# Optimization experiments

Measured on AMD Instinct MI355X. Metric: run time of the kernel, lower is better.

## Reference

```python
import jax, jax.numpy as jnp
import numpy as np

SCALE = 1.0 / 4.0      # alpha / dim
MULTIPLIER = 1.0

def _act(h):
    return jax.nn.gelu(h, approximate=False)  # torch nn.GELU(approximate='none')

def setup_inputs() -> dict:
    key = jax.random.key(0)
    ks = jax.random.split(key, 9)
    B, T, D = 64, 77, 768
    N, R = 1024, 4
    return {
        "x":     jax.random.normal(ks[0], (B, T, D), jnp.float32),
        "W_org": jax.random.normal(ks[1], (D, D), jnp.float32) * 0.02,
        "b_org": jax.random.normal(ks[2], (D,), jnp.float32) * 0.02,
        "w1":    jax.random.normal(ks[3], (N, D, R), jnp.float32) * 0.02,
        "b1":    jax.random.normal(ks[4], (N, R), jnp.float32) * 0.02,
        "mid_w": jax.random.normal(ks[5], (N, R, R), jnp.float32) * 0.02,
        "mid_b": jax.random.normal(ks[6], (N, R), jnp.float32) * 0.02,
        "w_out": jax.random.normal(ks[7], (N, R, D), jnp.float32) * 0.02,
        "b_out": jax.random.normal(ks[8], (N, D), jnp.float32) * 0.02,
    }

def reference(x, W_org, b_org, w1, b1, mid_w, mid_b, w_out, b_out):
    # per-concept low-rank MLP: h in [B, T, N, R]
    h = jnp.einsum('btd,ndh->btnh', x, w1) + b1[None, None]
    h = _act(h)
    # repeated 'h' in 'nhh' takes the diagonal of mid_w (elementwise scale),
    # exactly matching torch.einsum semantics in the source.
    h = jnp.einsum('btnh,nhh->btnh', h, mid_w) + mid_b[None, None]
    h = _act(h)
    # fuse out-projection with sum over concepts: sum_n (h_n @ w_out_n) + sum_n b_out_n
    up = jnp.einsum('btnh,nhd->btd', h, w_out) + jnp.sum(b_out, axis=0)
    org = x @ W_org.T + b_org
    return org + up * (MULTIPLIER * SCALE)
```

## Files before the change

### kernel.cpp

```cpp
#include <hip/hip_runtime.h>
#include <hip/hip_bf16.h>

#define M_TOK 4928
#define M_PAD 5120
#define D_DIM 768
#define NR    4096
#define K_CAT 4864
#define KT_ALL 152

typedef __bf16 bf16;
typedef __attribute__((ext_vector_type(8))) __bf16 bf16x8;
typedef __attribute__((ext_vector_type(4))) float f32x4;
typedef __attribute__((address_space(1))) uint32_t gu32;
typedef __attribute__((address_space(3))) uint32_t su32;

__device__ __forceinline__ float gelu_fast(float v) {
  float p = v * v;
  float u = v * fmaf(0.07135481283f, p, 1.595769122f);
  float e = __expf(-u);
  return v * __builtin_amdgcn_rcpf(1.0f + e);
}

__device__ __forceinline__ int xcd_swizzle(int orig, int nwg) {
  const int q = nwg >> 3, r = nwg & 7;
  const int x = orig & 7, rest = orig >> 3;
  return (x < r ? x * (q + 1) : r * (q + 1) + (x - r) * q) + rest;
}


__global__ __launch_bounds__(256) void k_prep_x(const float* __restrict__ x,
                                                bf16* __restrict__ Xb) {
  int idx = (blockIdx.x * 256 + threadIdx.x) * 4;
  if (idx >= M_PAD * D_DIM) return;
  int m = idx / D_DIM;
  union { uint2 u; bf16 h[4]; } o;
  if (m < M_TOK) {
    float4 v = *(const float4*)(x + idx);
    o.h[0] = (bf16)v.x; o.h[1] = (bf16)v.y; o.h[2] = (bf16)v.z; o.h[3] = (bf16)v.w;
  } else {
    o.h[0] = o.h[1] = o.h[2] = o.h[3] = (bf16)0.0f;
  }
  *(uint2*)(Xb + idx) = o.u;
}

__global__ __launch_bounds__(256) void k_prep_w1t(const float* __restrict__ w1,
                                                  bf16* __restrict__ W1t) {
  int idx = (blockIdx.x * 256 + threadIdx.x) * 4;
  if (idx >= NR * D_DIM) return;
  int j = idx / D_DIM, d0 = idx % D_DIM;
  int n = j >> 2, r = j & 3;
  const float* src = w1 + n * (D_DIM * 4) + r;
  union { uint2 u; bf16 h[4]; } o;
#pragma unroll
  for (int i = 0; i < 4; ++i) o.h[i] = (bf16)src[(d0 + i) * 4];
  *(uint2*)(W1t + idx) = o.u;
}

__global__ __launch_bounds__(256) void k_prep_w2t_t(const float* __restrict__ w_out,
                                                    bf16* __restrict__ W2t) {
  __shared__ float S[64 * 65];
  const int bk = blockIdx.x & 63, bd = blockIdx.x >> 6;
  const int k0 = bk * 64, d0 = bd * 64;
  const int tr = threadIdx.x >> 4;
  const int tc = (threadIdx.x & 15) * 4;
#pragma unroll
  for (int p = 0; p < 4; ++p) {
    const int kr = tr + p * 16;
    float4 v = *(const float4*)(w_out + (size_t)(k0 + kr) * D_DIM + d0 + tc);
    S[kr * 65 + tc + 0] = v.x; S[kr * 65 + tc + 1] = v.y;
    S[kr * 65 + tc + 2] = v.z; S[kr * 65 + tc + 3] = v.w;
  }
  __syncthreads();
#pragma unroll
  for (int p = 0; p < 4; ++p) {
    const int dr = tr + p * 16;
    union { uint2 u; bf16 h[4]; } o;
#pragma unroll
    for (int i = 0; i < 4; ++i) o.h[i] = (bf16)(0.25f * S[(tc + i) * 65 + dr]);
    *(uint2*)(W2t + (size_t)(d0 + dr) * K_CAT + k0 + tc) = o.u;
  }
}

__global__ __launch_bounds__(256) void k_prep_w2t_org(const float* __restrict__ W_org,
                                                      bf16* __restrict__ W2t) {
  int idx = (blockIdx.x * 256 + threadIdx.x) * 4;
  if (idx >= D_DIM * D_DIM) return;
  int d = idx / D_DIM, c = idx % D_DIM;
  float4 v = *(const float4*)(W_org + idx);
  union { uint2 u; bf16 h[4]; } o;
  o.h[0] = (bf16)v.x; o.h[1] = (bf16)v.y; o.h[2] = (bf16)v.z; o.h[3] = (bf16)v.w;
  *(uint2*)(W2t + (size_t)d * K_CAT + NR + c) = o.u;
}

__global__ __launch_bounds__(256) void k_bias_partial(const float* __restrict__ b_out,
                                                      float* __restrict__ partial) {
  int b = blockIdx.x;
  for (int d = threadIdx.x; d < D_DIM; d += 256) {
    float s = 0.0f;
    for (int n = b * 32; n < b * 32 + 32; ++n) s += b_out[n * D_DIM + d];
    partial[b * D_DIM + d] = s;
  }
}

__global__ __launch_bounds__(256) void k_bias_final(const float* __restrict__ partial,
                                                    const float* __restrict__ b_org,
                                                    float* __restrict__ bias_total) {
  int d = blockIdx.x * 256 + threadIdx.x;
  if (d >= D_DIM) return;
  float s = 0.0f;
#pragma unroll
  for (int b = 0; b < 32; ++b) s += partial[b * D_DIM + d];
  bias_total[d] = b_org[d] + 0.25f * s;
}


__device__ __forceinline__ int swz_slot(int kg, int lr) {
  return (kg ^ ((lr >> 1) & 3)) << 3;
}

__device__ __forceinline__ void stage_tile4(const bf16* g, int ld, int row0, int col0,
                                            bf16* lds) {
  const int lane = threadIdx.x & 63;
  const int wave = threadIdx.x >> 6;
  const int src_slot = (lane & 3) ^ ((lane >> 3) & 3);
#pragma unroll
  for (int c = 0; c < 2; ++c) {
    const int chunk = wave * 2 + c;
    const int row = row0 + chunk * 16 + (lane >> 2);
    const bf16* gp = g + (size_t)row * ld + col0 + (src_slot << 3);
    __builtin_amdgcn_global_load_lds((gu32*)gp, (su32*)(lds + chunk * 512), 16, 0, 0);
  }
}

__device__ __forceinline__ void stage_unit8(const bf16* g, int ld, int row0, int col0,
                                            bf16* lds) {
  const int lane = threadIdx.x & 63;
  const int wave = threadIdx.x >> 6;
  const int src_slot = (lane & 3) ^ ((lane >> 3) & 3);
#pragma unroll
  for (int c = 0; c < 2; ++c) {
    const int chunk = wave * 2 + c;
    const int row = row0 + chunk * 16 + (lane >> 2);
    const bf16* gp = g + (size_t)row * ld + col0 + (src_slot << 3);
    __builtin_amdgcn_global_load_lds((gu32*)gp, (su32*)(lds + chunk * 512), 16, 0, 0);
  }
}

#define TILE_E (128 * 32)

#define PIPE_LOOP(KT0, KT1, STAGE_PAIR, BODY)                                   \
  {                                                                             \
    STAGE_PAIR(KT0, 0);                                                         \
    STAGE_PAIR((KT0) + 1, 1);                                                   \
    int ra = 0;                                                                 \
    for (int kt = (KT0); kt < (KT1); ++kt) {                                    \
      if (kt + 1 < (KT1)) { asm volatile("s_waitcnt vmcnt(4)" ::: "memory"); }  \
      else                { asm volatile("s_waitcnt vmcnt(0)" ::: "memory"); }  \
      asm volatile("s_barrier" ::: "memory");                                   \
      const int rs = ra + 2 >= 3 ? ra - 1 : ra + 2;                             \
      BODY(ra);                                                                 \
      if (kt + 2 < (KT1)) STAGE_PAIR(kt + 2, rs);                               \
      ra = (ra + 1 == 3) ? 0 : ra + 1;                                          \
    }                                                                           \
  }

__global__ __launch_bounds__(256) void k_gemm1(const bf16* __restrict__ Xb,
                                               const bf16* __restrict__ W1t,
                                               bf16* __restrict__ H2,
                                               const float* __restrict__ b1,
                                               const float* __restrict__ midw,
                                               const float* __restrict__ midb) {
  __shared__ bf16 As[3][TILE_E];
  __shared__ bf16 Bs[3][TILE_E];
  const int wgid = xcd_swizzle(blockIdx.x, 40 * 32);
  const int bmt = wgid >> 5;
  const int bnt = wgid & 31;
  const int m0 = bmt * 128, n0 = bnt * 128;
  const int lane = threadIdx.x & 63;
  const int wave = threadIdx.x >> 6;
  const int wm = wave >> 1, wn = wave & 1;
  const int lr = lane & 15, kg = lane >> 4;
  const int slot = swz_slot(kg, lr);

  f32x4 acc[4][4];
#pragma unroll
  for (int i = 0; i < 4; ++i)
#pragma unroll
    for (int j = 0; j < 4; ++j) acc[i][j] = (f32x4)(0.0f);

#define G1_STAGE(kt, buf)                                   \
  {                                                         \
    stage_tile4(Xb, D_DIM, m0, (kt) * 32, As[(buf)]);       \
    stage_tile4(W1t, D_DIM, n0, (kt) * 32, Bs[(buf)]);      \
  }
#define G1_BODY(cur)                                                         \
  {                                                                          \
    bf16x8 a[4], b[4];                                                       \
    _Pragma("unroll") for (int i = 0; i < 4; ++i)                            \
      a[i] = *(const bf16x8*)(As[(cur)] + (wm * 64 + i * 16 + lr) * 32 + slot); \
    _Pragma("unroll") for (int j = 0; j < 4; ++j)                            \
      b[j] = *(const bf16x8*)(Bs[(cur)] + (wn * 64 + j * 16 + lr) * 32 + slot); \
    _Pragma("unroll") for (int i = 0; i < 4; ++i)                            \
      _Pragma("unroll") for (int j = 0; j < 4; ++j)                          \
        acc[i][j] = __builtin_amdgcn_mfma_f32_16x16x32_bf16(a[i], b[j], acc[i][j], 0, 0, 0); \
  }

  PIPE_LOOP(0, 24, G1_STAGE, G1_BODY)
#undef G1_STAGE
#undef G1_BODY

#pragma unroll
  for (int j = 0; j < 4; ++j) {
    const int col = n0 + wn * 64 + j * 16 + lr;
    const float b1v = b1[col];
    const float mdv = midw[(col >> 2) * 16 + (col & 3) * 5];
    const float mbv = midb[col];
#pragma unroll
    for (int i = 0; i < 4; ++i) {
      const int r0 = m0 + wm * 64 + i * 16 + kg * 4;
#pragma unroll
      for (int rr = 0; rr < 4; ++rr) {
        float h = acc[i][j][rr] + b1v;
        h = gelu_fast(h);
        h = h * mdv + mbv;
        h = gelu_fast(h);
        H2[(size_t)(r0 + rr) * NR + col] = (bf16)h;
      }
    }
  }
}


#define ENGINE(KT0, KT1, STAGE_A, STAGE_B)                                      \
  {                                                                             \
    STAGE_A((KT0) + 0, 0); STAGE_B((KT0) + 0, 0);                               \
    STAGE_A((KT0) + 1, 1); STAGE_B((KT0) + 1, 1);                               \
    STAGE_A((KT0) + 2, 2); STAGE_B((KT0) + 2, 2);                               \
    asm volatile("s_waitcnt vmcnt(8)" ::: "memory");                            \
    asm volatile("s_barrier" ::: "memory");                                     \
    for (int t = (KT0); t < (KT1); ++t) {                                       \
      const int s  = (t - (KT0)) & 3;                                           \
      const int st = (t - (KT0) + 3) & 3;                                       \
      const bool more = (t + 3 < (KT1));                                        \
      bf16x8 a[8], b[4];                                                        \
      _Pragma("unroll") for (int i = 0; i < 4; ++i)                             \
        a[i] = *(const bf16x8*)(As[s] + aBase + i * 512);                       \
      _Pragma("unroll") for (int j = 0; j < 4; ++j)                             \
        b[j] = *(const bf16x8*)(Bs[s] + bBase + j * 512);                       \
      if (more) { STAGE_A(t + 3, st); }                                         \
      asm volatile("s_barrier" ::: "memory");                                   \
      __builtin_amdgcn_s_setprio(1);                                            \
      _Pragma("unroll") for (int i = 0; i < 4; ++i)                             \
        _Pragma("unroll") for (int j = 0; j < 4; ++j)                           \
          acc[i][j] = __builtin_amdgcn_mfma_f32_16x16x32_bf16(a[i], b[j], acc[i][j], 0, 0, 0); \
      __builtin_amdgcn_s_setprio(0);                                            \
      asm volatile("s_barrier" ::: "memory");                                   \
      _Pragma("unroll") for (int i = 0; i < 4; ++i)                             \
        a[4 + i] = *(const bf16x8*)(As[s] + aBase + 2048 + i * 512);            \
      if (more) { STAGE_B(t + 3, st); }                                         \
      {                                                                         \
        int ahead = ((KT1) - 1) - (t + 1);                                      \
        if (ahead >= 2)      { asm volatile("s_waitcnt vmcnt(8)" ::: "memory"); } \
        else if (ahead == 1) { asm volatile("s_waitcnt vmcnt(4)" ::: "memory"); } \
        else                 { asm volatile("s_waitcnt vmcnt(0)" ::: "memory"); } \
      }                                                                         \
      asm volatile("s_barrier" ::: "memory");                                   \
      __builtin_amdgcn_s_setprio(1);                                            \
      _Pragma("unroll") for (int i = 0; i < 4; ++i)                             \
        _Pragma("unroll") for (int j = 0; j < 4; ++j)                           \
          acc[4 + i][j] = __builtin_amdgcn_mfma_f32_16x16x32_bf16(a[4 + i], b[j], acc[4 + i][j], 0, 0, 0); \
      __builtin_amdgcn_s_setprio(0);                                            \
      asm volatile("s_barrier" ::: "memory");                                   \
    }                                                                           \
  }

template <int SPLITS>
__global__ __launch_bounds__(512) void k_gemm2(const bf16* __restrict__ H2,
                                               const bf16* __restrict__ Xb,
                                               const bf16* __restrict__ W2t,
                                               void* __restrict__ outp,
                                               const float* __restrict__ bias) {
  __shared__ bf16 As[4][8192];
  __shared__ bf16 Bs[4][8192];
  const int nwg = 20 * 3 * SPLITS;
  const int wgid = xcd_swizzle(blockIdx.x, nwg);
  const int bmt = wgid / (3 * SPLITS);
  const int rem = wgid % (3 * SPLITS);
  const int ks  = rem / 3;
  const int bnt = rem % 3;
  const int m0 = bmt * 256, n0 = bnt * 256;
  const int lane = threadIdx.x & 63;
  const int wave = threadIdx.x >> 6;
  const int wm = wave >> 2, wn = wave & 3;
  const int lr = lane & 15, kg = lane >> 4;
  const int slotE = swz_slot(kg, lr);
  const int aBase = (wm * 128 + lr) * 32 + slotE;
  const int bBase = (wn * 64 + lr) * 32 + slotE;
  constexpr int KT_PER = KT_ALL / SPLITS;
  const int kt0 = ks * KT_PER, kt1 = kt0 + KT_PER;

  f32x4 acc[8][4];
#pragma unroll
  for (int i = 0; i < 8; ++i)
#pragma unroll
    for (int j = 0; j < 4; ++j) acc[i][j] = (f32x4)(0.0f);

#define G2_SA(kt, buf)                                                  \
  {                                                                     \
    const int k0s = (kt) * 32;                                          \
    if (k0s < NR) stage_unit8(H2, NR, m0, k0s, As[(buf)]);              \
    else          stage_unit8(Xb, D_DIM, m0, k0s - NR, As[(buf)]);      \
  }
#define G2_SB(kt, buf) stage_unit8(W2t, K_CAT, n0, (kt) * 32, Bs[(buf)])
  ENGINE(kt0, kt1, G2_SA, G2_SB)
#undef G2_SA
#undef G2_SB

  if (SPLITS > 1) {
    bf16* dst = (bf16*)outp + (size_t)ks * M_TOK * D_DIM;
#pragma unroll
    for (int j = 0; j < 4; ++j) {
      const int col = n0 + wn * 64 + j * 16 + lr;
#pragma unroll
      for (int i = 0; i < 8; ++i) {
        const int r0 = m0 + wm * 128 + i * 16 + kg * 4;
#pragma unroll
        for (int rr = 0; rr < 4; ++rr) {
          const int row = r0 + rr;
          if (row < M_TOK) dst[(size_t)row * D_DIM + col] = (bf16)acc[i][j][rr];
        }
      }
    }
  } else {
    float* dst = (float*)outp;
#pragma unroll
    for (int j = 0; j < 4; ++j) {
      const int col = n0 + wn * 64 + j * 16 + lr;
      const float bv = bias[col];
#pragma unroll
      for (int i = 0; i < 8; ++i) {
        const int r0 = m0 + wm * 128 + i * 16 + kg * 4;
#pragma unroll
        for (int rr = 0; rr < 4; ++rr) {
          const int row = r0 + rr;
          if (row < M_TOK) dst[(size_t)row * D_DIM + col] = acc[i][j][rr] + bv;
        }
      }
    }
  }
}

template <int SPLITS>
__global__ __launch_bounds__(256) void k_reduce(const bf16* __restrict__ padd,
                                                const float* __restrict__ bias,
                                                float* __restrict__ out) {
  int idx = (blockIdx.x * 256 + threadIdx.x) * 4;
  if (idx >= M_TOK * D_DIM) return;
  float4 s = *(const float4*)(bias + (idx % D_DIM));
#pragma unroll
  for (int p = 0; p < SPLITS; ++p) {
    union { uint2 u; bf16 h[4]; } v;
    v.u = *(const uint2*)(padd + (size_t)p * M_TOK * D_DIM + idx);
    s.x += (float)v.h[0]; s.y += (float)v.h[1];
    s.z += (float)v.h[2]; s.w += (float)v.h[3];
  }
  *(float4*)(out + idx) = s;
}


extern "C" void kernel_launch(void* const* d_in, const int* in_sizes, int n_in,
                              void* d_out, int out_size, void* d_ws, size_t ws_size,
                              hipStream_t stream) {
  const float* x     = (const float*)d_in[0];
  const float* W_org = (const float*)d_in[1];
  const float* b_org = (const float*)d_in[2];
  const float* w1    = (const float*)d_in[3];
  const float* b1    = (const float*)d_in[4];
  const float* mid_w = (const float*)d_in[5];
  const float* mid_b = (const float*)d_in[6];
  const float* w_out = (const float*)d_in[7];
  const float* b_out = (const float*)d_in[8];
  float* out = (float*)d_out;

  bf16* Xb   = (bf16*)d_ws;
  bf16* W1t  = Xb  + (size_t)M_PAD * D_DIM;
  bf16* W2t  = W1t + (size_t)NR * D_DIM;
  bf16* H2   = W2t + (size_t)D_DIM * K_CAT;
  float* bias    = (float*)(H2 + (size_t)M_PAD * NR);
  float* partial = bias + 1024;
  bf16* padd     = (bf16*)(partial + 32 * D_DIM);

  const size_t base_bytes = (size_t)((char*)padd - (char*)d_ws);
  const size_t per_split  = (size_t)M_TOK * D_DIM * sizeof(bf16);
  int S = 1;
  if (ws_size >= base_bytes + 4 * per_split)      S = 4;
  else if (ws_size >= base_bytes + 2 * per_split) S = 2;

  k_prep_x     <<<(M_PAD * D_DIM / 4) / 256, 256, 0, stream>>>(x, Xb);
  k_prep_w1t   <<<(NR * D_DIM / 4) / 256, 256, 0, stream>>>(w1, W1t);
  k_prep_w2t_t <<<64 * 12, 256, 0, stream>>>(w_out, W2t);
  k_prep_w2t_org<<<(D_DIM * D_DIM / 4 + 255) / 256, 256, 0, stream>>>(W_org, W2t);
  k_bias_partial<<<32, 256, 0, stream>>>(b_out, partial);
  k_bias_final  <<<3, 256, 0, stream>>>(partial, b_org, bias);

  k_gemm1<<<40 * 32, 256, 0, stream>>>(Xb, W1t, H2, b1, mid_w, mid_b);

  const int red_grid = (M_TOK * D_DIM / 4 + 255) / 256;
  if (S == 4) {
    k_gemm2<4><<<20 * 3 * 4, 512, 0, stream>>>(H2, Xb, W2t, padd, bias);
    k_reduce<4><<<red_grid, 256, 0, stream>>>(padd, bias, out);
  } else if (S == 2) {
    k_gemm2<2><<<20 * 3 * 2, 512, 0, stream>>>(H2, Xb, W2t, padd, bias);
    k_reduce<2><<<red_grid, 256, 0, stream>>>(padd, bias, out);
  } else {
    k_gemm2<1><<<20 * 3, 512, 0, stream>>>(H2, Xb, W2t, out, bias);
  }
}
```

Baseline: 136.6 us.

## Restructure GEMM2 main loop to 64-wide K tiles with double buffering

Replaces the 4-stage, 32-wide-K pipeline in the second GEMM with a 2-stage pipeline over 64-wide K tiles, using a new staging routine and an XOR swizzle adapted to 64-element rows. Each iteration now issues four MFMA groups per tile and prefetches two tiles ahead into the buffer just consumed. This halves the number of loop iterations and the barrier and wait overhead per unit of K, but gives less prefetch depth and adds more barriers inside each iteration. The split count must divide 76 tiles.

Measured after the change: 137.5 us. Within noise of the previous version (+0.7%).

```diff
diff --git a/kernel.cpp b/kernel.cpp
--- a/kernel.cpp
+++ b/kernel.cpp
@@ -7,6 +7,7 @@
 #define NR    4096
 #define K_CAT 4864
 #define KT_ALL 152
+#define NT64_ALL 76
 
 typedef __bf16 bf16;
 typedef __attribute__((ext_vector_type(8))) __bf16 bf16x8;
@@ -119,20 +120,6 @@
 }
 
 __device__ __forceinline__ void stage_tile4(const bf16* g, int ld, int row0, int col0,
-                                            bf16* lds) {
-  const int lane = threadIdx.x & 63;
-  const int wave = threadIdx.x >> 6;
-  const int src_slot = (lane & 3) ^ ((lane >> 3) & 3);
-#pragma unroll
-  for (int c = 0; c < 2; ++c) {
-    const int chunk = wave * 2 + c;
-    const int row = row0 + chunk * 16 + (lane >> 2);
-    const bf16* gp = g + (size_t)row * ld + col0 + (src_slot << 3);
-    __builtin_amdgcn_global_load_lds((gu32*)gp, (su32*)(lds + chunk * 512), 16, 0, 0);
-  }
-}
-
-__device__ __forceinline__ void stage_unit8(const bf16* g, int ld, int row0, int col0,
                                             bf16* lds) {
   const int lane = threadIdx.x & 63;
   const int wave = threadIdx.x >> 6;
@@ -231,48 +218,20 @@
 }
 
 
-#define ENGINE(KT0, KT1, STAGE_A, STAGE_B)                                      \
-  {                                                                             \
-    STAGE_A((KT0) + 0, 0); STAGE_B((KT0) + 0, 0);                               \
-    STAGE_A((KT0) + 1, 1); STAGE_B((KT0) + 1, 1);                               \
-    STAGE_A((KT0) + 2, 2); STAGE_B((KT0) + 2, 2);                               \
-    asm volatile("s_waitcnt vmcnt(8)" ::: "memory");                            \
-    asm volatile("s_barrier" ::: "memory");                                     \
-    for (int t = (KT0); t < (KT1); ++t) {                                       \
-      const int s  = (t - (KT0)) & 3;                                           \
-      const int st = (t - (KT0) + 3) & 3;                                       \
-      const bool more = (t + 3 < (KT1));                                        \
-      bf16x8 a[8], b[4];                                                        \
-      _Pragma("unroll") for (int i = 0; i < 4; ++i)                             \
-        a[i] = *(const bf16x8*)(As[s] + aBase + i * 512);                       \
-      _Pragma("unroll") for (int j = 0; j < 4; ++j)                             \
-        b[j] = *(const bf16x8*)(Bs[s] + bBase + j * 512);                       \
-      if (more) { STAGE_A(t + 3, st); }                                         \
-      asm volatile("s_barrier" ::: "memory");                                   \
-      __builtin_amdgcn_s_setprio(1);                                            \
-      _Pragma("unroll") for (int i = 0; i < 4; ++i)                             \
-        _Pragma("unroll") for (int j = 0; j < 4; ++j)                           \
-          acc[i][j] = __builtin_amdgcn_mfma_f32_16x16x32_bf16(a[i], b[j], acc[i][j], 0, 0, 0); \
-      __builtin_amdgcn_s_setprio(0);                                            \
-      asm volatile("s_barrier" ::: "memory");                                   \
-      _Pragma("unroll") for (int i = 0; i < 4; ++i)                             \
-        a[4 + i] = *(const bf16x8*)(As[s] + aBase + 2048 + i * 512);            \
-      if (more) { STAGE_B(t + 3, st); }                                         \
-      {                                                                         \
-        int ahead = ((KT1) - 1) - (t + 1);                                      \
-        if (ahead >= 2)      { asm volatile("s_waitcnt vmcnt(8)" ::: "memory"); } \
-        else if (ahead == 1) { asm volatile("s_waitcnt vmcnt(4)" ::: "memory"); } \
-        else                 { asm volatile("s_waitcnt vmcnt(0)" ::: "memory"); } \
-      }                                                                         \
-      asm volatile("s_barrier" ::: "memory");                                   \
-      __builtin_amdgcn_s_setprio(1);                                            \
-      _Pragma("unroll") for (int i = 0; i < 4; ++i)                             \
-        _Pragma("unroll") for (int j = 0; j < 4; ++j)                           \
-          acc[4 + i][j] = __builtin_amdgcn_mfma_f32_16x16x32_bf16(a[4 + i], b[j], acc[4 + i][j], 0, 0, 0); \
-      __builtin_amdgcn_s_setprio(0);                                            \
-      asm volatile("s_barrier" ::: "memory");                                   \
-    }                                                                           \
-  }
+__device__ __forceinline__ void stage64(const bf16* g, int ld, int row0, int col0,
+                                        bf16* lds) {
+  const int lane = threadIdx.x & 63;
+  const int wave = threadIdx.x >> 6;
+  const int rsub = lane >> 3;
+  const int src_slot = (lane & 7) ^ rsub;
+#pragma unroll
+  for (int c = 0; c < 4; ++c) {
+    const int chunk = wave * 4 + c;
+    const int row = row0 + chunk * 8 + rsub;
+    const bf16* gp = g + (size_t)row * ld + col0 + (src_slot << 3);
+    __builtin_amdgcn_global_load_lds((gu32*)gp, (su32*)(lds + chunk * 512), 16, 0, 0);
+  }
+}
 
 template <int SPLITS>
 __global__ __launch_bounds__(512) void k_gemm2(const bf16* __restrict__ H2,
@@ -280,8 +239,8 @@
                                                const bf16* __restrict__ W2t,
                                                void* __restrict__ outp,
                                                const float* __restrict__ bias) {
-  __shared__ bf16 As[4][8192];
-  __shared__ bf16 Bs[4][8192];
+  __shared__ bf16 As[2][256 * 64];
+  __shared__ bf16 Bs[2][256 * 64];
   const int nwg = 20 * 3 * SPLITS;
   const int wgid = xcd_swizzle(blockIdx.x, nwg);
   const int bmt = wgid / (3 * SPLITS);
@@ -293,11 +252,11 @@
   const int wave = threadIdx.x >> 6;
   const int wm = wave >> 2, wn = wave & 3;
   const int lr = lane & 15, kg = lane >> 4;
-  const int slotE = swz_slot(kg, lr);
-  const int aBase = (wm * 128 + lr) * 32 + slotE;
-  const int bBase = (wn * 64 + lr) * 32 + slotE;
-  constexpr int KT_PER = KT_ALL / SPLITS;
-  const int kt0 = ks * KT_PER, kt1 = kt0 + KT_PER;
+  const int c0  = lr * 64 + ((kg ^ (lr & 7)) << 3);
+  const int aB0 = wm * 8192 + c0;
+  const int bB0 = wn * 4096 + c0;
+  constexpr int NT = NT64_ALL / SPLITS;
+  const int t0 = ks * NT;
 
   f32x4 acc[8][4];
 #pragma unroll
@@ -305,14 +264,77 @@
 #pragma unroll
     for (int j = 0; j < 4; ++j) acc[i][j] = (f32x4)(0.0f);
 
-#define G2_SA(kt, buf)                                                  \
+#define G2_SA(t, s)                                                     \
   {                                                                     \
-    const int k0s = (kt) * 32;                                          \
-    if (k0s < NR) stage_unit8(H2, NR, m0, k0s, As[(buf)]);              \
-    else          stage_unit8(Xb, D_DIM, m0, k0s - NR, As[(buf)]);      \
-  }
-#define G2_SB(kt, buf) stage_unit8(W2t, K_CAT, n0, (kt) * 32, Bs[(buf)])
-  ENGINE(kt0, kt1, G2_SA, G2_SB)
+    const int k0s = (t0 + (t)) * 64;                                    \
+    if (k0s < NR) stage64(H2, NR, m0, k0s, As[(s)]);                    \
+    else          stage64(Xb, D_DIM, m0, k0s - NR, As[(s)]);            \
+  }
+#define G2_SB(t, s) stage64(W2t, K_CAT, n0, (t0 + (t)) * 64, Bs[(s)])
+
+  G2_SA(0, 0); G2_SB(0, 0);
+  G2_SA(1, 1); G2_SB(1, 1);
+
+  for (int t = 0; t < NT; ++t) {
+    const int s = t & 1;
+    const bf16* Ap = As[s];
+    const bf16* Bp = Bs[s];
+    if (t + 1 < NT) { asm volatile("s_waitcnt vmcnt(8)" ::: "memory"); }
+    else            { asm volatile("s_waitcnt vmcnt(0)" ::: "memory"); }
+    asm volatile("s_barrier" ::: "memory");
+
+    bf16x8 a[4], b[4];
+#pragma unroll
+    for (int i = 0; i < 4; ++i) a[i] = *(const bf16x8*)(Ap + aB0 + i * 1024);
+#pragma unroll
+    for (int j = 0; j < 4; ++j) b[j] = *(const bf16x8*)(Bp + bB0 + j * 1024);
+    asm volatile("s_barrier" ::: "memory");
+    __builtin_amdgcn_s_setprio(1);
+#pragma unroll
+    for (int i = 0; i < 4; ++i)
+#pragma unroll
+      for (int j = 0; j < 4; ++j)
+        acc[i][j] = __builtin_amdgcn_mfma_f32_16x16x32_bf16(a[i], b[j], acc[i][j], 0, 0, 0);
+    __builtin_amdgcn_s_setprio(0);
+    asm volatile("s_barrier" ::: "memory");
+#pragma unroll
+    for (int i = 0; i < 4; ++i) a[i] = *(const bf16x8*)(Ap + aB0 + (4 + i) * 1024);
+    asm volatile("s_barrier" ::: "memory");
+    __builtin_amdgcn_s_setprio(1);
+#pragma unroll
+    for (int i = 0; i < 4; ++i)
+#pragma unroll
+      for (int j = 0; j < 4; ++j)
+        acc[4 + i][j] = __builtin_amdgcn_mfma_f32_16x16x32_bf16(a[i], b[j], acc[4 + i][j], 0, 0, 0);
+    __builtin_amdgcn_s_setprio(0);
+    asm volatile("s_barrier" ::: "memory");
+#pragma unroll
+    for (int i = 0; i < 4; ++i) a[i] = *(const bf16x8*)(Ap + (aB0 ^ 32) + i * 1024);
+#pragma unroll
+    for (int j = 0; j < 4; ++j) b[j] = *(const bf16x8*)(Bp + (bB0 ^ 32) + j * 1024);
+    asm volatile("s_barrier" ::: "memory");
+    __builtin_amdgcn_s_setprio(1);
+#pragma unroll
+    for (int i = 0; i < 4; ++i)
+#pragma unroll
+      for (int j = 0; j < 4; ++j)
+        acc[i][j] = __builtin_amdgcn_mfma_f32_16x16x32_bf16(a[i], b[j], acc[i][j], 0, 0, 0);
+    __builtin_amdgcn_s_setprio(0);
+    asm volatile("s_barrier" ::: "memory");
+#pragma unroll
+    for (int i = 0; i < 4; ++i) a[i] = *(const bf16x8*)(Ap + ((aB0 ^ 32) + (4 + i) * 1024));
+    asm volatile("s_waitcnt lgkmcnt(0)" ::: "memory");
+    asm volatile("s_barrier" ::: "memory");
+    if (t + 2 < NT) { G2_SA(t + 2, s); G2_SB(t + 2, s); }
+    __builtin_amdgcn_s_setprio(1);
+#pragma unroll
+    for (int i = 0; i < 4; ++i)
+#pragma unroll
+      for (int j = 0; j < 4; ++j)
+        acc[4 + i][j] = __builtin_amdgcn_mfma_f32_16x16x32_bf16(a[i], b[j], acc[4 + i][j], 0, 0, 0);
+    __builtin_amdgcn_s_setprio(0);
+    asm volatile("s_barrier" ::: "memory");
+  }
 #undef G2_SA
 #undef G2_SB
 
```
